# Performance work log

Measured on AMD Instinct MI355X. Metric: run time of the kernel, lower is better.

Reference implementation:

```python
import jax, jax.numpy as jnp
import numpy as np

N, G, E, H, OUT, MAX_N = 131072, 256, 384, 6, 256, 1024
DH = E // H  # 64


def _make_sizes():
    # variable-length segments summing exactly to N, each in [1, MAX_N]
    rng = np.random.default_rng(0)
    raw = rng.integers(128, 896, G).astype(np.int64)
    diff = int(N - raw.sum())
    q, r = divmod(diff, G)
    sizes = raw + q
    sizes[:r] += 1
    assert sizes.sum() == N and sizes.min() >= 1 and sizes.max() <= MAX_N
    return sizes


def setup_inputs() -> dict:
    key = jax.random.key(0)
    ks = jax.random.split(key, 8)
    s = 1.0 / np.sqrt(E)
    return {
        "node_feat": jax.random.normal(ks[0], (N, E), jnp.float32),
        "sizes": jnp.asarray(_make_sizes(), jnp.int32),
        "query": jax.random.normal(ks[1], (E,), jnp.float32),
        "Wq": jax.random.normal(ks[2], (E, E), jnp.float32) * s,
        "bq": jnp.zeros((E,), jnp.float32),
        "Wk": jax.random.normal(ks[3], (E, E), jnp.float32) * s,
        "bk": jnp.zeros((E,), jnp.float32),
        "Wv": jax.random.normal(ks[4], (E, E), jnp.float32) * s,
        "bv": jnp.zeros((E,), jnp.float32),
        "Wo": jax.random.normal(ks[5], (E, E), jnp.float32) * s,
        "bo": jnp.zeros((E,), jnp.float32),
        "Wp": jax.random.normal(ks[6], (OUT, E), jnp.float32) * s,
        "bp": jnp.zeros((OUT,), jnp.float32),
    }


def reference(node_feat, sizes, query, Wq, bq, Wk, bk, Wv, bv, Wo, bo, Wp, bp):
    # segment offsets and padded gather indices
    offsets = jnp.cumsum(sizes) - sizes                      # [G]
    pos = jnp.arange(MAX_N)
    idx = jnp.clip(offsets[:, None] + pos[None, :], 0, N - 1)  # [G, MAX_N]
    mask = pos[None, :] < sizes[:, None]                     # [G, MAX_N]

    # project K/V on the flat node table (one big GEMM), then gather into padded form
    k_flat = node_feat @ Wk.T + bk                           # [N, E]
    v_flat = node_feat @ Wv.T + bv
    k = k_flat[idx].reshape(G, MAX_N, H, DH)
    v = v_flat[idx].reshape(G, MAX_N, H, DH)

    # single shared query token, pre-scaled (PyTorch MHA scales q by 1/sqrt(head_dim))
    q = ((query @ Wq.T + bq) * (1.0 / np.sqrt(DH))).reshape(H, DH)

    scores = jnp.einsum('hd,gnhd->ghn', q, k)                # [G, H, MAX_N]
    scores = jnp.where(mask[:, None, :], scores, -1e30)
    attn = jax.nn.softmax(scores, axis=-1)
    pooled = jnp.einsum('ghn,gnhd->ghd', attn, v).reshape(G, E)

    out = pooled @ Wo.T + bo                                 # MHA out_proj
    return out @ Wp.T + bp                                   # final proj  [G, OUT]
```

## Files before the change

kernel.cpp:

```cpp
#include <hip/hip_runtime.h>
#include <math.h>

#define NN 131072
#define G  256
#define E  384
#define H  6
#define DH 64
#define OUTD 256
#define MAXN 1024

#define WS_QK   0
#define WS_C    2304
#define WS_OFF  2432
#define WS_QV   2944
#define WS_WVT  12288
#define WS_WOT  (WS_WVT + E*E)
#define WS_WPT  (WS_WOT + E*E)

__global__ __launch_bounds__(256) void k0a_scan_qv(
    const int* __restrict__ sizes, const float* __restrict__ query,
    const float* __restrict__ Wq, const float* __restrict__ bq,
    float* __restrict__ wsf) {
  const int tid = threadIdx.x;
  if (blockIdx.x == 0) {
    __shared__ int s_scan[G];
    const int sz = sizes[tid];
    s_scan[tid] = sz;
    __syncthreads();
    for (int d = 1; d < G; d <<= 1) {
      int t = (tid >= d) ? s_scan[tid - d] : 0;
      __syncthreads();
      s_scan[tid] += t;
      __syncthreads();
    }
    ((int*)(wsf + WS_OFF))[tid] = s_scan[tid] - sz;
  } else {
    const int lane = tid & 63;
    const int i = (blockIdx.x - 1) * 4 + (tid >> 6);
    float a = 0.f;
#pragma unroll
    for (int j = 0; j < 6; j++)
      a += Wq[(size_t)i * E + j * 64 + lane] * query[j * 64 + lane];
#pragma unroll
    for (int mm = 1; mm < 64; mm <<= 1) a += __shfl_xor(a, mm, 64);
    if (lane == 0) wsf[WS_QV + i] = 0.125f * (a + bq[i]);
  }
}

__global__ __launch_bounds__(256) void k0b_qk(
    const float* __restrict__ Wk, const float* __restrict__ bk,
    float* __restrict__ wsf) {
  __shared__ float qv_s[64];
  __shared__ float ps[256];
  const int h = blockIdx.x / 6, ec = blockIdx.x % 6;
  const int tid = threadIdx.x;
  if (tid < 64) qv_s[tid] = wsf[WS_QV + h * 64 + tid];
  __syncthreads();
  const int el = tid & 63, dq = tid >> 6;
  float a = 0.f;
#pragma unroll 4
  for (int d = dq * 16; d < dq * 16 + 16; d++)
    a += qv_s[d] * Wk[(size_t)(h * 64 + d) * E + ec * 64 + el];
  ps[tid] = a;
  __syncthreads();
  if (tid < 64)
    wsf[WS_QK + h * E + ec * 64 + tid] =
        ps[tid] + ps[64 + tid] + ps[128 + tid] + ps[192 + tid];
}

__global__ __launch_bounds__(256) void k0t_transpose(
    const float* __restrict__ Wv, const float* __restrict__ Wo,
    const float* __restrict__ Wp, float* __restrict__ wsf) {
  __shared__ float s[64][65];
  const int b = blockIdx.x;
  const float* src;
  float* dst;
  int R, tr, tc;
  if (b < 36)      { src = Wv; dst = wsf + WS_WVT; R = 384; tr = b / 6;        tc = b % 6; }
  else if (b < 72) { src = Wo; dst = wsf + WS_WOT; R = 384; tr = (b - 36) / 6; tc = (b - 36) % 6; }
  else             { src = Wp; dst = wsf + WS_WPT; R = 256; tr = (b - 72) / 6; tc = (b - 72) % 6; }
  const int r0 = tr * 64, c0 = tc * 64;
#pragma unroll
  for (int k = 0; k < 16; k++) {
    int idx = k * 256 + threadIdx.x;
    int r = idx >> 6, cc = idx & 63;
    s[r][cc] = src[(size_t)(r0 + r) * E + c0 + cc];
  }
  __syncthreads();
#pragma unroll
  for (int k = 0; k < 16; k++) {
    int idx = k * 256 + threadIdx.x;
    int cc = idx >> 6, r = idx & 63;
    dst[(size_t)(c0 + cc) * R + r0 + r] = s[r][cc];
  }
}

template <int CTRL>
__device__ __forceinline__ float dpp_radd(float v) {
  int t = __builtin_amdgcn_update_dpp(0, __float_as_int(v), CTRL, 0xf, 0xf, true);
  return v + __int_as_float(t);
}
__device__ __forceinline__ float wave_sum64(float v) {
  v = dpp_radd<0xB1>(v);
  v = dpp_radd<0x4E>(v);
  v = dpp_radd<0x141>(v);
  v = dpp_radd<0x140>(v);
  v += __shfl_xor(v, 16, 64);
  v += __shfl_xor(v, 32, 64);
  return v;
}

__global__ __launch_bounds__(768, 3) void k12g_fused(
    const float* __restrict__ x, const int* __restrict__ sizes,
    const float* __restrict__ bv, const float* __restrict__ bo,
    const float* __restrict__ bp, float* __restrict__ out,
    const float* __restrict__ wsf) {
  __shared__ float xsl[4][H * E];
  __shared__ float ps[768];
  __shared__ float pooled[E];
  __shared__ float om[E];
  __shared__ float msh[12][H], lsh[12][H], wgts[12][H];
  __shared__ float linv[H];

  const int tid = threadIdx.x;
  const int lane = tid & 63;
  const int w = tid >> 6;
  const int g = blockIdx.x;
  const int sz = sizes[g];
  const int n0 = ((const int*)(wsf + WS_OFF))[g];

  float qk[6][6];
#pragma unroll
  for (int h = 0; h < 6; h++)
#pragma unroll
    for (int k = 0; k < 6; k++) qk[h][k] = wsf[WS_QK + h * E + k * 64 + lane];

  float m[6], l[6], acc[6][6];
#pragma unroll
  for (int h = 0; h < 6; h++) {
    m[h] = -3.0e38f;
    l[h] = 0.f;
#pragma unroll
    for (int k = 0; k < 6; k++) acc[h][k] = 0.f;
  }

  const float* xp = x + (size_t)(n0 + w) * E + lane;
  const int cnt = (sz > w) ? ((sz - w + 11) / 12) : 0;

  float x0[6], x1[6];
#define LOADX(buf, i)                                              \
  {                                                                \
    const float* p_ = xp + (size_t)(i) * (12 * E);                 \
    _Pragma("unroll") for (int k_ = 0; k_ < 6; k_++)               \
        buf[k_] = p_[k_ * 64];                                     \
  }
#define COMPUTE(xv)                                                          \
  {                                                                          \
    float sr[6];                                                             \
    _Pragma("unroll") for (int h_ = 0; h_ < 6; h_++) {                       \
      float a_ = qk[h_][0] * xv[0];                                          \
      _Pragma("unroll") for (int k_ = 1; k_ < 6; k_++)                       \
          a_ = fmaf(qk[h_][k_], xv[k_], a_);                                 \
      sr[h_] = a_;                                                           \
    }                                                                        \
    _Pragma("unroll") for (int h_ = 0; h_ < 6; h_++)                         \
        sr[h_] = wave_sum64(sr[h_]);                                         \
    bool upd_ = false;                                                       \
    _Pragma("unroll") for (int h_ = 0; h_ < 6; h_++)                         \
        upd_ = upd_ || (sr[h_] > m[h_] + 8.0f);                              \
    if (upd_) {                                                              \
      _Pragma("unroll") for (int h_ = 0; h_ < 6; h_++) {                     \
        const float nm_ = fmaxf(m[h_], sr[h_]);                              \
        const float f_ = __expf(m[h_] - nm_);                                \
        m[h_] = nm_;                                                         \
        l[h_] *= f_;                                                         \
        _Pragma("unroll") for (int k_ = 0; k_ < 6; k_++) acc[h_][k_] *= f_;  \
      }                                                                      \
    }                                                                        \
    _Pragma("unroll") for (int h_ = 0; h_ < 6; h_++) {                       \
      const float p_ = __expf(sr[h_] - m[h_]);                               \
      l[h_] += p_;                                                           \
      _Pragma("unroll") for (int k_ = 0; k_ < 6; k_++)                       \
          acc[h_][k_] = fmaf(p_, xv[k_], acc[h_][k_]);                       \
    }                                                                        \
  }

  if (cnt > 0) {
    LOADX(x0, 0);
    int i = 0;
    while (true) {
      int ip = (i + 1 < cnt) ? i + 1 : i;
      LOADX(x1, ip);
      COMPUTE(x0);
      if (++i >= cnt) break;
      ip = (i + 1 < cnt) ? i + 1 : i;
      LOADX(x0, ip);
      COMPUTE(x1);
      if (++i >= cnt) break;
    }
  }
#undef LOADX
#undef COMPUTE

  if (lane == 0) {
#pragma unroll
    for (int h = 0; h < 6; h++) {
      msh[w][h] = m[h];
      lsh[w][h] = l[h];
    }
  }
  __syncthreads();
  if (tid < 6) {
    const int h = tid;
    float M = -3.0e38f;
    for (int s = 0; s < 12; s++) M = fmaxf(M, msh[s][h]);
    float L = 0.f;
    for (int s = 0; s < 12; s++) {
      const float wv_ = __expf(msh[s][h] - M);
      wgts[s][h] = wv_;
      L += lsh[s][h] * wv_;
    }
    linv[h] = 1.0f / L;
  }
  __syncthreads();
  {
    float wg[6];
#pragma unroll
    for (int h = 0; h < 6; h++) wg[h] = wgts[w][h];
#pragma unroll
    for (int h = 0; h < 6; h++)
#pragma unroll
      for (int k = 0; k < 6; k++) acc[h][k] *= wg[h];
  }
  {
    float* xs = &xsl[w & 3][0];
    if (w < 4) {
#pragma unroll
      for (int h = 0; h < 6; h++)
#pragma unroll
        for (int k = 0; k < 6; k++) xs[h * E + k * 64 + lane] = acc[h][k];
    }
    __syncthreads();
    if (w >= 4 && w < 8) {
#pragma unroll
      for (int h = 0; h < 6; h++)
#pragma unroll
        for (int k = 0; k < 6; k++) xs[h * E + k * 64 + lane] += acc[h][k];
    }
    __syncthreads();
    if (w >= 8) {
#pragma unroll
      for (int h = 0; h < 6; h++)
#pragma unroll
        for (int k = 0; k < 6; k++) xs[h * E + k * 64 + lane] += acc[h][k];
    }
    __syncthreads();
  }
  for (int idx = tid; idx < H * E; idx += 768) {
    const int h = idx / E;
    xsl[0][idx] = ((xsl[0][idx] + xsl[1][idx]) + (xsl[2][idx] + xsl[3][idx]))
                  * linv[h];
  }
  __syncthreads();

  const float* xb = &xsl[0][0];
  const float* wvt = wsf + WS_WVT;
  const float* wot = wsf + WS_WOT;
  const float* wpt = wsf + WS_WPT;

  {
    const int i = tid % 384, ks = tid / 384;
    const float* xh = xb + (i >> 6) * E + ks * 192;
    const float* wp_ = wvt + (size_t)(ks * 192) * E + i;
    float a0 = 0.f, a1 = 0.f, a2 = 0.f, a3 = 0.f;
#pragma unroll 4
    for (int e = 0; e < 192; e += 4) {
      a0 += wp_[(size_t)(e + 0) * E] * xh[e + 0];
      a1 += wp_[(size_t)(e + 1) * E] * xh[e + 1];
      a2 += wp_[(size_t)(e + 2) * E] * xh[e + 2];
      a3 += wp_[(size_t)(e + 3) * E] * xh[e + 3];
    }
    ps[tid] = (a0 + a1) + (a2 + a3);
  }
  __syncthreads();
  if (tid < 384) pooled[tid] = ps[tid] + ps[384 + tid] + bv[tid];
  __syncthreads();

  {
    const int i = tid % 384, ks = tid / 384;
    const float* xh = pooled + ks * 192;
    const float* wp_ = wot + (size_t)(ks * 192) * E + i;
    float a0 = 0.f, a1 = 0.f, a2 = 0.f, a3 = 0.f;
#pragma unroll 4
    for (int e = 0; e < 192; e += 4) {
      a0 += wp_[(size_t)(e + 0) * E] * xh[e + 0];
      a1 += wp_[(size_t)(e + 1) * E] * xh[e + 1];
      a2 += wp_[(size_t)(e + 2) * E] * xh[e + 2];
      a3 += wp_[(size_t)(e + 3) * E] * xh[e + 3];
    }
    ps[tid] = (a0 + a1) + (a2 + a3);
  }
  __syncthreads();
  if (tid < 384) om[tid] = ps[tid] + ps[384 + tid] + bo[tid];
  __syncthreads();

  {
    const int o = tid % 256, ks = tid / 256;
    const float* xh = om + ks * 128;
    const float* wp_ = wpt + (size_t)(ks * 128) * OUTD + o;
    float a0 = 0.f, a1 = 0.f, a2 = 0.f, a3 = 0.f;
#pragma unroll 4
    for (int e = 0; e < 128; e += 4) {
      a0 += wp_[(size_t)(e + 0) * OUTD] * xh[e + 0];
      a1 += wp_[(size_t)(e + 1) * OUTD] * xh[e + 1];
      a2 += wp_[(size_t)(e + 2) * OUTD] * xh[e + 2];
      a3 += wp_[(size_t)(e + 3) * OUTD] * xh[e + 3];
    }
    ps[tid] = (a0 + a1) + (a2 + a3);
  }
  __syncthreads();
  if (tid < 256)
    out[(size_t)g * OUTD + tid] = ps[tid] + ps[256 + tid] + ps[512 + tid] + bp[tid];
}

extern "C" void kernel_launch(void* const* d_in, const int* in_sizes, int n_in,
                              void* d_out, int out_size, void* d_ws, size_t ws_size,
                              hipStream_t stream) {
  const float* x     = (const float*)d_in[0];
  const int*   sizes = (const int*)d_in[1];
  const float* query = (const float*)d_in[2];
  const float* Wq    = (const float*)d_in[3];
  const float* bq    = (const float*)d_in[4];
  const float* Wk    = (const float*)d_in[5];
  const float* bk    = (const float*)d_in[6];
  const float* Wv    = (const float*)d_in[7];
  const float* bv    = (const float*)d_in[8];
  const float* Wo    = (const float*)d_in[9];
  const float* bo    = (const float*)d_in[10];
  const float* Wp    = (const float*)d_in[11];
  const float* bp    = (const float*)d_in[12];
  float* wsf = (float*)d_ws;
  float* out = (float*)d_out;

  hipLaunchKernelGGL(k0a_scan_qv, dim3(97), dim3(256), 0, stream,
                     sizes, query, Wq, bq, wsf);
  hipLaunchKernelGGL(k0b_qk, dim3(36), dim3(256), 0, stream, Wk, bk, wsf);
  hipLaunchKernelGGL(k0t_transpose, dim3(96), dim3(256), 0, stream,
                     Wv, Wo, Wp, wsf);
  hipLaunchKernelGGL(k12g_fused, dim3(G), dim3(768), 0, stream,
                     x, sizes, bv, bo, bp, out, wsf);
}
```

Baseline: 338.9 us.

## Merge prep kernels, widen fused kernel to 16 waves with vector loads and triple buffering

Folds the scan, query-projection, qk and transpose kernels into a single prep launch, with each qk block recomputing its own slice of the projected query. The main kernel moves from 12 to 16 waves per block, switches row loads to float4/float2 with a permuted column mapping, and prefetches two rows ahead with three buffers. This aims to cut launch overhead and raise memory-level parallelism in the bandwidth-bound node scan. The cost is redundant Wq work across qk blocks, more registers, and a 1024-thread block that may limit occupancy.

Result: slower. 969.6 us (+186.1%).

```diff
diff --git a/kernel.cpp b/kernel.cpp
--- a/kernel.cpp
+++ b/kernel.cpp
@@ -10,19 +10,20 @@
 #define MAXN 1024
 
 #define WS_QK   0
-#define WS_C    2304
 #define WS_OFF  2432
-#define WS_QV   2944
 #define WS_WVT  12288
 #define WS_WOT  (WS_WVT + E*E)
 #define WS_WPT  (WS_WOT + E*E)
 
-__global__ __launch_bounds__(256) void k0a_scan_qv(
+__global__ __launch_bounds__(256) void k_prep(
     const int* __restrict__ sizes, const float* __restrict__ query,
     const float* __restrict__ Wq, const float* __restrict__ bq,
+    const float* __restrict__ Wk, const float* __restrict__ Wv,
+    const float* __restrict__ Wo, const float* __restrict__ Wp,
     float* __restrict__ wsf) {
+  const int b = blockIdx.x;
   const int tid = threadIdx.x;
-  if (blockIdx.x == 0) {
+  if (b == 0) {
     __shared__ int s_scan[G];
     const int sz = sizes[tid];
     s_scan[tid] = sz;
@@ -34,64 +35,59 @@
       __syncthreads();
     }
     ((int*)(wsf + WS_OFF))[tid] = s_scan[tid] - sz;
+  } else if (b <= 36) {
+    const int h = (b - 1) / 6, ec = (b - 1) % 6;
+    __shared__ float qv_s[64];
+    __shared__ float qps[256];
+    __shared__ float ps[256];
+    {
+      const int r = tid >> 2, q = tid & 3;
+      const int row = h * 64 + r;
+      float a = 0.f;
+#pragma unroll 4
+      for (int j = 0; j < 96; j++)
+        a += Wq[(size_t)row * E + q * 96 + j] * query[q * 96 + j];
+      qps[tid] = a;
+    }
+    __syncthreads();
+    if (tid < 64)
+      qv_s[tid] = 0.125f * (qps[tid * 4] + qps[tid * 4 + 1] +
+                            qps[tid * 4 + 2] + qps[tid * 4 + 3] +
+                            bq[h * 64 + tid]);
+    __syncthreads();
+    const int el = tid & 63, dq = tid >> 6;
+    float a = 0.f;
+#pragma unroll 4
+    for (int d = dq * 16; d < dq * 16 + 16; d++)
+      a += qv_s[d] * Wk[(size_t)(h * 64 + d) * E + ec * 64 + el];
+    ps[tid] = a;
+    __syncthreads();
+    if (tid < 64)
+      wsf[WS_QK + h * E + ec * 64 + tid] =
+          ps[tid] + ps[64 + tid] + ps[128 + tid] + ps[192 + tid];
   } else {
-    const int lane = tid & 63;
-    const int i = (blockIdx.x - 1) * 4 + (tid >> 6);
-    float a = 0.f;
-#pragma unroll
-    for (int j = 0; j < 6; j++)
-      a += Wq[(size_t)i * E + j * 64 + lane] * query[j * 64 + lane];
-#pragma unroll
-    for (int mm = 1; mm < 64; mm <<= 1) a += __shfl_xor(a, mm, 64);
-    if (lane == 0) wsf[WS_QV + i] = 0.125f * (a + bq[i]);
-  }
-}
-
-__global__ __launch_bounds__(256) void k0b_qk(
-    const float* __restrict__ Wk, const float* __restrict__ bk,
-    float* __restrict__ wsf) {
-  __shared__ float qv_s[64];
-  __shared__ float ps[256];
-  const int h = blockIdx.x / 6, ec = blockIdx.x % 6;
-  const int tid = threadIdx.x;
-  if (tid < 64) qv_s[tid] = wsf[WS_QV + h * 64 + tid];
-  __syncthreads();
-  const int el = tid & 63, dq = tid >> 6;
-  float a = 0.f;
-#pragma unroll 4
-  for (int d = dq * 16; d < dq * 16 + 16; d++)
-    a += qv_s[d] * Wk[(size_t)(h * 64 + d) * E + ec * 64 + el];
-  ps[tid] = a;
-  __syncthreads();
-  if (tid < 64)
-    wsf[WS_QK + h * E + ec * 64 + tid] =
-        ps[tid] + ps[64 + tid] + ps[128 + tid] + ps[192 + tid];
-}
-
-__global__ __launch_bounds__(256) void k0t_transpose(
-    const float* __restrict__ Wv, const float* __restrict__ Wo,
-    const float* __restrict__ Wp, float* __restrict__ wsf) {
-  __shared__ float s[64][65];
-  const int b = blockIdx.x;
-  const float* src;
-  float* dst;
-  int R, tr, tc;
-  if (b < 36)      { src = Wv; dst = wsf + WS_WVT; R = 384; tr = b / 6;        tc = b % 6; }
-  else if (b < 72) { src = Wo; dst = wsf + WS_WOT; R = 384; tr = (b - 36) / 6; tc = (b - 36) % 6; }
-  else             { src = Wp; dst = wsf + WS_WPT; R = 256; tr = (b - 72) / 6; tc = (b - 72) % 6; }
-  const int r0 = tr * 64, c0 = tc * 64;
-#pragma unroll
-  for (int k = 0; k < 16; k++) {
-    int idx = k * 256 + threadIdx.x;
-    int r = idx >> 6, cc = idx & 63;
-    s[r][cc] = src[(size_t)(r0 + r) * E + c0 + cc];
-  }
-  __syncthreads();
-#pragma unroll
-  for (int k = 0; k < 16; k++) {
-    int idx = k * 256 + threadIdx.x;
-    int cc = idx >> 6, r = idx & 63;
-    dst[(size_t)(c0 + cc) * R + r0 + r] = s[r][cc];
+    __shared__ float s[64][65];
+    const int t = b - 37;
+    const float* src;
+    float* dst;
+    int R, tr, tc;
+    if (t < 36)      { src = Wv; dst = wsf + WS_WVT; R = 384; tr = t / 6;        tc = t % 6; }
+    else if (t < 72) { src = Wo; dst = wsf + WS_WOT; R = 384; tr = (t - 36) / 6; tc = (t - 36) % 6; }
+    else             { src = Wp; dst = wsf + WS_WPT; R = 256; tr = (t - 72) / 6; tc = (t - 72) % 6; }
+    const int r0 = tr * 64, c0 = tc * 64;
+#pragma unroll
+    for (int k = 0; k < 16; k++) {
+      int idx = k * 256 + tid;
+      int r = idx >> 6, cc = idx & 63;
+      s[r][cc] = src[(size_t)(r0 + r) * E + c0 + cc];
+    }
+    __syncthreads();
+#pragma unroll
+    for (int k = 0; k < 16; k++) {
+      int idx = k * 256 + tid;
+      int cc = idx >> 6, r = idx & 63;
+      dst[(size_t)(c0 + cc) * R + r0 + r] = s[r][cc];
+    }
   }
 }
 
@@ -110,7 +106,7 @@
   return v;
 }
 
-__global__ __launch_bounds__(768, 3) void k12g_fused(
+__global__ __launch_bounds__(1024, 4) void k12g_fused(
     const float* __restrict__ x, const int* __restrict__ sizes,
     const float* __restrict__ bv, const float* __restrict__ bo,
     const float* __restrict__ bp, float* __restrict__ out,
@@ -119,7 +115,7 @@
   __shared__ float ps[768];
   __shared__ float pooled[E];
   __shared__ float om[E];
-  __shared__ float msh[12][H], lsh[12][H], wgts[12][H];
+  __shared__ float msh[16][H], lsh[16][H], wgts[16][H];
   __shared__ float linv[H];
 
   const int tid = threadIdx.x;
@@ -131,9 +127,12 @@
 
   float qk[6][6];
 #pragma unroll
-  for (int h = 0; h < 6; h++)
-#pragma unroll
-    for (int k = 0; k < 6; k++) qk[h][k] = wsf[WS_QK + h * E + k * 64 + lane];
+  for (int h = 0; h < 6; h++) {
+    const float4 q4 = *(const float4*)&wsf[WS_QK + h * E + 4 * lane];
+    const float2 q2 = *(const float2*)&wsf[WS_QK + h * E + 256 + 2 * lane];
+    qk[h][0] = q4.x; qk[h][1] = q4.y; qk[h][2] = q4.z; qk[h][3] = q4.w;
+    qk[h][4] = q2.x; qk[h][5] = q2.y;
+  }
 
   float m[6], l[6], acc[6][6];
 #pragma unroll
@@ -144,15 +143,17 @@
     for (int k = 0; k < 6; k++) acc[h][k] = 0.f;
   }
 
-  const float* xp = x + (size_t)(n0 + w) * E + lane;
-  const int cnt = (sz > w) ? ((sz - w + 11) / 12) : 0;
-
-  float x0[6], x1[6];
+  const float* xp = x + (size_t)(n0 + w) * E;
+  const int cnt = (sz > w) ? ((sz - w + 15) / 16) : 0;
+
+  float x0[6], x1[6], x2[6];
 #define LOADX(buf, i)                                              \
   {                                                                \
-    const float* p_ = xp + (size_t)(i) * (12 * E);                 \
-    _Pragma("unroll") for (int k_ = 0; k_ < 6; k_++)               \
-        buf[k_] = p_[k_ * 64];                                     \
+    const float* p_ = xp + (size_t)(i) * (16 * E);                 \
+    const float4 v4_ = *(const float4*)(p_ + 4 * lane);            \
+    const float2 v2_ = *(const float2*)(p_ + 256 + 2 * lane);      \
+    buf[0] = v4_.x; buf[1] = v4_.y; buf[2] = v4_.z; buf[3] = v4_.w;\
+    buf[4] = v2_.x; buf[5] = v2_.y;                                \
   }
 #define COMPUTE(xv)                                                          \
   {                                                                          \
@@ -187,15 +188,20 @@
 
   if (cnt > 0) {
     LOADX(x0, 0);
+    {
+      const int i1 = (1 < cnt) ? 1 : (cnt - 1);
+      LOADX(x1, i1);
+    }
     int i = 0;
     while (true) {
-      int ip = (i + 1 < cnt) ? i + 1 : i;
-      LOADX(x1, ip);
+      { const int ip = (i + 2 < cnt) ? i + 2 : cnt - 1; LOADX(x2, ip); }
       COMPUTE(x0);
       if (++i >= cnt) break;
-      ip = (i + 1 < cnt) ? i + 1 : i;
-      LOADX(x0, ip);
+      { const int ip = (i + 2 < cnt) ? i + 2 : cnt - 1; LOADX(x0, ip); }
       COMPUTE(x1);
+      if (++i >= cnt) break;
+      { const int ip = (i + 2 < cnt) ? i + 2 : cnt - 1; LOADX(x1, ip); }
+      COMPUTE(x2);
       if (++i >= cnt) break;
     }
   }
@@ -213,9 +219,9 @@
   if (tid < 6) {
     const int h = tid;
     float M = -3.0e38f;
-    for (int s = 0; s < 12; s++) M = fmaxf(M, msh[s][h]);
+    for (int s = 0; s < 16; s++) M = fmaxf(M, msh[s][h]);
     float L = 0.f;
-    for (int s = 0; s < 12; s++) {
+    for (int s = 0; s < 16; s++) {
       const float wv_ = __expf(msh[s][h] - M);
       wgts[s][h] = wv_;
       L += lsh[s][h] * wv_;
@@ -236,27 +242,46 @@
     float* xs = &xsl[w & 3][0];
     if (w < 4) {
 #pragma unroll
-      for (int h = 0; h < 6; h++)
-#pragma unroll
-        for (int k = 0; k < 6; k++) xs[h * E + k * 64 + lane] = acc[h][k];
+      for (int h = 0; h < 6; h++) {
+#pragma unroll
+        for (int k = 0; k < 4; k++) xs[h * E + 4 * lane + k] = acc[h][k];
+#pragma unroll
+        for (int k = 4; k < 6; k++) xs[h * E + 256 + 2 * lane + (k - 4)] = acc[h][k];
+      }
     }
     __syncthreads();
     if (w >= 4 && w < 8) {
 #pragma unroll
-      for (int h = 0; h < 6; h++)
-#pragma unroll
-        for (int k = 0; k < 6; k++) xs[h * E + k * 64 + lane] += acc[h][k];
-    }
-    __syncthreads();
-    if (w >= 8) {
-#pragma unroll
-      for (int h = 0; h < 6; h++)
-#pragma unroll
-        for (int k = 0; k < 6; k++) xs[h * E + k * 64 + lane] += acc[h][k];
-    }
-    __syncthreads();
-  }
-  for (int idx = tid; idx < H * E; idx += 768) {
+      for (int h = 0; h < 6; h++) {
+#pragma unroll
+        for (int k = 0; k < 4; k++) xs[h * E + 4 * lane + k] += acc[h][k];
+#pragma unroll
+        for (int k = 4; k < 6; k++) xs[h * E + 256 + 2 * lane + (k - 4)] += acc[h][k];
+      }
+    }
+    __syncthreads();
+    if (w >= 8 && w < 12) {
+#pragma unroll
+      for (int h = 0; h < 6; h++) {
+#pragma unroll
+        for (int k = 0; k < 4; k++) xs[h * E + 4 * lane + k] += acc[h][k];
+#pragma unroll
+        for (int k = 4; k < 6; k++) xs[h * E + 256 + 2 * lane + (k - 4)] += acc[h][k];
+      }
+    }
+    __syncthreads();
+    if (w >= 12) {
+#pragma unroll
+      for (int h = 0; h < 6; h++) {
+#pragma unroll
+        for (int k = 0; k < 4; k++) xs[h * E + 4 * lane + k] += acc[h][k];
+#pragma unroll
+        for (int k = 4; k < 6; k++) xs[h * E + 256 + 2 * lane + (k - 4)] += acc[h][k];
+      }
+    }
+    __syncthreads();
+  }
+  for (int idx = tid; idx < H * E; idx += 1024) {
     const int h = idx / E;
     xsl[0][idx] = ((xsl[0][idx] + xsl[1][idx]) + (xsl[2][idx] + xsl[3][idx]))
                   * linv[h];
@@ -268,7 +293,7 @@
   const float* wot = wsf + WS_WOT;
   const float* wpt = wsf + WS_WPT;
 
-  {
+  if (tid < 768) {
     const int i = tid % 384, ks = tid / 384;
     const float* xh = xb + (i >> 6) * E + ks * 192;
     const float* wp_ = wvt + (size_t)(ks * 192) * E + i;
@@ -286,7 +311,7 @@
   if (tid < 384) pooled[tid] = ps[tid] + ps[384 + tid] + bv[tid];
   __syncthreads();
 
-  {
+  if (tid < 768) {
     const int i = tid % 384, ks = tid / 384;
     const float* xh = pooled + ks * 192;
     const float* wp_ = wot + (size_t)(ks * 192) * E + i;
@@ -304,7 +329,7 @@
   if (tid < 384) om[tid] = ps[tid] + ps[384 + tid] + bo[tid];
   __syncthreads();
 
-  {
+  if (tid < 768) {
     const int o = tid % 256, ks = tid / 256;
     const float* xh = om + ks * 128;
     const float* wp_ = wpt + (size_t)(ks * 128) * OUTD + o;
@@ -332,7 +357,7 @@
   const float* Wq    = (const float*)d_in[3];
   const float* bq    = (const float*)d_in[4];
   const float* Wk    = (const float*)d_in[5];
-  const float* bk    = (const float*)d_in[6];
+  const float* bk    = (const float*)d_in[6];  (void)bk;
   const float* Wv    = (const float*)d_in[7];
   const float* bv    = (const float*)d_in[8];
   const float* Wo    = (const float*)d_in[9];
@@ -342,11 +367,8 @@
   float* wsf = (float*)d_ws;
   float* out = (float*)d_out;
 
-  hipLaunchKernelGGL(k0a_scan_qv, dim3(97), dim3(256), 0, stream,
-                     sizes, query, Wq, bq, wsf);
-  hipLaunchKernelGGL(k0b_qk, dim3(36), dim3(256), 0, stream, Wk, bk, wsf);
-  hipLaunchKernelGGL(k0t_transpose, dim3(96), dim3(256), 0, stream,
-                     Wv, Wo, Wp, wsf);
-  hipLaunchKernelGGL(k12g_fused, dim3(G), dim3(768), 0, stream,
+  hipLaunchKernelGGL(k_prep, dim3(133), dim3(256), 0, stream,
+                     sizes, query, Wq, bq, Wk, Wv, Wo, Wp, wsf);
+  hipLaunchKernelGGL(k12g_fused, dim3(G), dim3(1024), 0, stream,
                      x, sizes, bv, bo, bp, out, wsf);
 }
```
